# Kernel tuning notes

Measured on AMD Instinct MI355X. Metric: run time of the kernel, lower is better.

The kernel has to match this reference:

```python
import jax, jax.numpy as jnp
import numpy as np

DIM = 512
NUM_ITEM = 2048
K = 10


def setup_inputs() -> dict:
    key = jax.random.key(0)
    k1, k2, k3 = jax.random.split(key, 3)
    input1 = jax.random.normal(k1, (16, DIM, 32, 32), dtype=jnp.float32)
    input2 = jax.random.normal(k2, (16, DIM, 32, 32), dtype=jnp.float32)
    stdv = 1.0 / np.sqrt(DIM)
    mempool = jax.random.uniform(k3, (NUM_ITEM, DIM), minval=-stdv, maxval=stdv, dtype=jnp.float32)
    return {"input1": input1, "input2": input2, "mempool": mempool}


def _memorize(x, mempool):
    # x: [B, C, H, W] with C == DIM
    B, C, H, W = x.shape
    q = jnp.transpose(x, (0, 2, 3, 1)).reshape(-1, C)      # [N, C]
    att = jax.nn.softmax(q @ mempool.T, axis=1)            # [N, num_item]
    val, idx = jax.lax.top_k(att, K)                       # [N, K]
    val = jax.nn.softmax(val, axis=1)                      # renormalize top-k
    # scatter(val into zeros) @ mempool == gather rows of mempool and combine
    out = jnp.einsum('nk,nkd->nd', val, mempool[idx])      # [N, C]
    return jnp.transpose(out.reshape(B, H, W, C), (0, 3, 1, 2))


def reference(input1, input2, mempool):
    return (_memorize(input1, mempool), _memorize(input2, mempool))
```

## Files before the change

### kernel.cpp

```cpp
#include <hip/hip_runtime.h>
#include <math.h>

typedef __attribute__((ext_vector_type(4))) float f4;
typedef __attribute__((ext_vector_type(8))) _Float16 f16x8;
typedef __attribute__((ext_vector_type(8))) short bf16x8;
typedef __attribute__((ext_vector_type(4))) unsigned short u16x4;
typedef unsigned int u32;
typedef unsigned short u16;

#define DIMC  512
#define NITEM 2048
#define TK    10
#define WSP   (NITEM * DIMC)
#define XWSP  (32 * DIMC * 1024)
#define QWS_OFF (3 * WSP)

#define TPB    512
#define PXB    64
#define RIT    256
#define NRND   8
#define NSLICE 16

#define SSTR   66
#define MV_F 0
#define MI_F 5120
#define MM_F 10240
#define MS_F 10752
#define WB_F 11264
#define IB_F 11904

#define QB_SZ  12288
#define Q_PL   4096
#define LDS_BYTES 67584
#define KSWZ(i) (((i) ^ ((i) >> 2)) & 3)

union h16 { _Float16 h; u16 u; };

__device__ __forceinline__ u32 bf16_rne(float f) {
    u32 u = __float_as_uint(f);
    return (u + 0x7fffu + ((u >> 16) & 1u)) >> 16;
}

__device__ __forceinline__ void split3(float f, u16& ph, u16& pb, u16& pr) {
    h16 a; a.h = (_Float16)f;
    float f0 = (float)a.h;
    ph = a.u;
    pb = (u16)bf16_rne(f);
    pr = (u16)bf16_rne(f - f0);
}

__global__ __launch_bounds__(256)
void preconv_kernel(const float* __restrict__ mp, u16* __restrict__ ws)
{
    int idx = (blockIdx.x * 256 + threadIdx.x) * 4;
    int i  = idx >> 9;
    int k0 = idx & 511;
    f4 v = *(const f4*)(mp + (size_t)i * 512 + k0);
    int s  = k0 >> 5, kl = k0 & 31;
    int lh = (kl >> 2) & 3, pair = kl >> 4;
    u16x4 pH, pB, pR;
#pragma unroll
    for (int e = 0; e < 4; ++e) {
        u16 h, b, r; split3(v[e], h, b, r);
        pH[e] = h; pB[e] = b; pR[e] = r;
    }
    size_t base = (size_t)(i >> 4) * 8192 + (size_t)s * 512
                + (size_t)(lh * 16 + (i & 15)) * 8 + pair * 4;
    *(u16x4*)(ws + 0 * WSP + base) = pH;
    *(u16x4*)(ws + 1 * WSP + base) = pB;
    *(u16x4*)(ws + 2 * WSP + base) = pR;
}

__global__ __launch_bounds__(256)
void preconv_x_kernel(const float* __restrict__ x0, const float* __restrict__ x1,
                      u16* __restrict__ ws)
{
    int T   = blockIdx.x * 256 + threadIdx.x;
    int px  = T & 1023;
    int c4  = (T >> 10) & 127;
    int img = T >> 17;
    const float* x = (img < 16) ? x0 : x1;
    const float* src = x + ((size_t)(img & 15) * 512 + (size_t)c4 * 4) * 1024 + px;
    int s = c4 >> 3, pair = (c4 >> 2) & 1, lh = c4 & 3;
    u16x4 pH, pB, pR;
#pragma unroll
    for (int j = 0; j < 4; ++j) {
        u16 h, b, r; split3(src[(size_t)j * 1024], h, b, r);
        pH[j] = h; pB[j] = b; pR[j] = r;
    }
    size_t base = (size_t)QWS_OFF
                + (size_t)(img * 64 + (px >> 4)) * 8192 + (size_t)s * 512
                + (size_t)((lh * 16 + (px & 15)) << 3) + pair * 4;
    *(u16x4*)(ws + base + 0 * (size_t)XWSP) = pH;
    *(u16x4*)(ws + base + 1 * (size_t)XWSP) = pB;
    *(u16x4*)(ws + base + 2 * (size_t)XWSP) = pR;
}

__global__ __launch_bounds__(TPB, 4)
void memorize_direct(const float* __restrict__ mp, const u16* __restrict__ ws,
                     float* __restrict__ out)
{
    __shared__ float ldsf[16896];

    const int t    = threadIdx.x;
    const int lane = t & 63;
    const int w    = t >> 6;
    const int blk  = blockIdx.x;
    const int img  = blk >> 4;
    const int n0   = (blk & 15) * PXB;

    float* ob = out + (img < 16 ? (size_t)0 : (size_t)16 * DIMC * 1024)
                    + (size_t)(img & 15) * (DIMC * 1024);

    const int l15 = lane & 15;
    const int lh  = lane >> 4;
    const int ig  = w >> 1;
    const int pg  = w & 1;

    const int qp = t & 63;
    const int g  = t >> 6;

    float tv[TK]; int tix[TK];
#pragma unroll
    for (int q = 0; q < TK; ++q) { tv[q] = -INFINITY; tix[q] = 0x7fffffff; }
    float rm = -INFINITY, rs = 0.0f;

    const u16* aw = ws + (size_t)lane * 8 + (size_t)(ig * 4) * 8192;
    const int G0 = img * 64 + (blk & 15) * 4 + pg * 2;
    const u16* bw = ws + (size_t)QWS_OFF + (size_t)G0 * 8192 + (size_t)lane * 8;

#define ALOAD(IT, S)                                                           \
    {                                                                          \
        const u16* ap = ar + ((size_t)(IT) << 13) + ((S) << 9);                \
        aH[IT] = *(const f16x8*) (ap + 0 * WSP);                               \
        aB[IT] = *(const bf16x8*)(ap + 1 * WSP);                               \
        aR[IT] = *(const bf16x8*)(ap + 2 * WSP);                               \
    }

#pragma unroll 1
    for (int r = 0; r < NRND; ++r) {
        const u16* ar = aw + ((size_t)r << 17);
        f4 acc[4][2];
#pragma unroll
        for (int it = 0; it < 4; ++it)
#pragma unroll
            for (int pt = 0; pt < 2; ++pt) acc[it][pt] = (f4){0.f, 0.f, 0.f, 0.f};

#pragma unroll 1
        for (int s = 0; s < NSLICE; ++s) {
            f16x8 qH[2]; bf16x8 qB[2], qR[2];
#pragma unroll
            for (int pt = 0; pt < 2; ++pt) {
                const u16* bp = bw + ((size_t)pt << 13) + ((size_t)s << 9);
                qH[pt] = *(const f16x8*) (bp + 0 * (size_t)XWSP);
                qB[pt] = *(const bf16x8*)(bp + 1 * (size_t)XWSP);
                qR[pt] = *(const bf16x8*)(bp + 2 * (size_t)XWSP);
            }
            f16x8 aH[4]; bf16x8 aB[4], aR[4];
            ALOAD(0, s)
            ALOAD(1, s)
#pragma unroll
            for (int it = 0; it < 4; ++it) {
                if (it < 2) ALOAD(it + 2, s)
#pragma unroll
                for (int pt = 0; pt < 2; ++pt) {
                    f4 c = acc[it][pt];
                    c = __builtin_amdgcn_mfma_f32_16x16x32_f16 (aH[it], qH[pt], c, 0, 0, 0);
                    c = __builtin_amdgcn_mfma_f32_16x16x32_bf16(aB[it], qR[pt], c, 0, 0, 0);
                    c = __builtin_amdgcn_mfma_f32_16x16x32_bf16(aR[it], qB[pt], c, 0, 0, 0);
                    acc[it][pt] = c;
                }
            }
        }

        __syncthreads();
#pragma unroll
        for (int it = 0; it < 4; ++it) {
#pragma unroll
            for (int pt = 0; pt < 2; ++pt) {
                int row = (ig << 6) + (it << 4) + (lh << 2);
                int col = (pg << 5) + (pt << 4) + l15;
                float* sp = ldsf + row * SSTR + col;
                sp[0 * SSTR] = acc[it][pt][0];
                sp[1 * SSTR] = acc[it][pt][1];
                sp[2 * SSTR] = acc[it][pt][2];
                sp[3 * SSTR] = acc[it][pt][3];
            }
        }
        __syncthreads();

        float mloc = rm;
#pragma unroll 4
        for (int jj = 0; jj < 32; ++jj) {
            int   il = (g << 5) + jj;
            float v  = ldsf[il * SSTR + qp];
            mloc = fmaxf(mloc, v);
            if (v > tv[TK - 1]) {
                int   id = r * RIT + il;
                float cv = v; int ci = id;
#pragma unroll
                for (int q = 0; q < TK; ++q) {
                    bool  gt = cv > tv[q];
                    float nv = gt ? tv[q]  : cv;
                    int   ni = gt ? tix[q] : ci;
                    tv[q]  = gt ? cv : tv[q];
                    tix[q] = gt ? ci : tix[q];
                    cv = nv; ci = ni;
                }
            }
        }
        rs *= __expf(rm - mloc);
        rm = mloc;
#pragma unroll 4
        for (int jj = 0; jj < 32; ++jj) {
            int   il = (g << 5) + jj;
            float v  = ldsf[il * SSTR + qp];
            rs += __expf(v - rm);
        }
    }
#undef ALOAD

    __syncthreads();
    {
#pragma unroll
        for (int q = 0; q < TK; ++q) {
            ldsf[MV_F + (qp * 8 + g) * TK + q] = tv[q];
            ldsf[MI_F + (qp * 8 + g) * TK + q] = __int_as_float(tix[q]);
        }
        ldsf[MM_F + qp * 8 + g] = rm;
        ldsf[MS_F + qp * 8 + g] = rs;
    }
    __syncthreads();

    if (t < 64) {
        const int p = t;
        float gm[8], gs[8];
#pragma unroll
        for (int G = 0; G < 8; ++G) {
            gm[G] = ldsf[MM_F + p * 8 + G];
            gs[G] = ldsf[MS_F + p * 8 + G];
        }
        float mstar = gm[0];
#pragma unroll
        for (int G = 1; G < 8; ++G) mstar = fmaxf(mstar, gm[G]);
        float Z = 0.0f;
#pragma unroll
        for (int G = 0; G < 8; ++G) Z += gs[G] * __expf(gm[G] - mstar);

        int h0=0,h1=0,h2=0,h3=0,h4=0,h5=0,h6=0,h7=0;
        float ov[TK]; int oi[TK];
#pragma unroll
        for (int o = 0; o < TK; ++o) {
            float bv = -INFINITY; int bi = 0x7fffffff; int bg = 0;
#define SEL(G, HG)                                                               \
            {                                                                    \
                float v  = ldsf[MV_F + (p * 8 + G) * TK + (HG)];                 \
                int   id = __float_as_int(ldsf[MI_F + (p * 8 + G) * TK + (HG)]); \
                if (v > bv || (v == bv && id < bi)) { bv = v; bi = id; bg = G; } \
            }
            SEL(0, h0) SEL(1, h1) SEL(2, h2) SEL(3, h3)
            SEL(4, h4) SEL(5, h5) SEL(6, h6) SEL(7, h7)
#undef SEL
            ov[o] = bv; oi[o] = bi;
            h0 += (bg == 0); h1 += (bg == 1); h2 += (bg == 2); h3 += (bg == 3);
            h4 += (bg == 4); h5 += (bg == 5); h6 += (bg == 6); h7 += (bg == 7);
        }
        float pv[TK];
#pragma unroll
        for (int o = 0; o < TK; ++o) pv[o] = __expf(ov[o] - mstar) / Z;
        float pmax = pv[0];
        float wgt[TK]; float W = 0.0f;
#pragma unroll
        for (int o = 0; o < TK; ++o) { wgt[o] = __expf(pv[o] - pmax); W += wgt[o]; }
#pragma unroll
        for (int o = 0; o < TK; ++o) {
            ldsf[WB_F + p * TK + o] = wgt[o] / W;
            ldsf[IB_F + p * TK + o] = __int_as_float(oi[o]);
        }
    }
    __syncthreads();

    {
        const int ep = t & 63, cg = t >> 6;
        float wr[TK]; const float* rows[TK];
#pragma unroll
        for (int o = 0; o < TK; ++o) {
            wr[o]   = ldsf[WB_F + ep * TK + o];
            rows[o] = mp + (size_t)__float_as_int(ldsf[IB_F + ep * TK + o]) * DIMC;
        }
        float* obase = ob + n0 + ep;
#pragma unroll 4
        for (int cc = 0; cc < 16; ++cc) {
            int c = cg * 64 + cc * 4;
            f4 a = {0.0f, 0.0f, 0.0f, 0.0f};
#pragma unroll
            for (int o = 0; o < TK; ++o) {
                f4 rv = *(const f4*)(rows[o] + c);
#pragma unroll
                for (int z = 0; z < 4; ++z) a[z] = fmaf(wr[o], rv[z], a[z]);
            }
#pragma unroll
            for (int z = 0; z < 4; ++z) obase[(size_t)(c + z) * 1024] = a[z];
        }
    }
}

__global__ __launch_bounds__(TPB, 4)
void memorize_fb(const float* __restrict__ x0, const float* __restrict__ x1,
                 const float* __restrict__ mp, const u16* __restrict__ ws,
                 float* __restrict__ out)
{
    extern __shared__ char ldsb[];
    float* ldsf = (float*)ldsb;

    const int t    = threadIdx.x;
    const int lane = t & 63;
    const int w    = t >> 6;
    const int blk  = blockIdx.x;
    const int img  = blk >> 4;
    const int n0   = (blk & 15) * PXB;
    const int b    = img & 15;

    const float* x  = (img < 16) ? x0 : x1;
    const float* xb = x + (size_t)b * (DIMC * 1024);
    float* ob = out + (img < 16 ? (size_t)0 : (size_t)16 * DIMC * 1024)
                    + (size_t)b * (DIMC * 1024);

    const int l15 = lane & 15;
    const int lh  = lane >> 4;
    const int ksw = lh ^ KSWZ(l15);
    const int ig  = w >> 1;
    const int pg  = w & 1;
    const int qp = t & 63;
    const int g  = t >> 6;

    float tv[TK]; int tix[TK];
#pragma unroll
    for (int q = 0; q < TK; ++q) { tv[q] = -INFINITY; tix[q] = 0x7fffffff; }
    float rm = -INFINITY, rs = 0.0f;

    const int scl  = t & 31;
    const int spx  = (t >> 5) << 2;
    const int spos = (((scl >> 2) & 3) << 3) + ((scl >> 4) << 2) + (scl & 3);
    const int sslot = spos >> 3;
    const int soff  = (spos & 7) << 1;

    const u16* aw = ws + (size_t)lane * 8 + (size_t)(ig * 4) * 8192;
    const int qfb = (pg << 11) + (l15 << 6) + (ksw << 4);

#define STAGE_Q(S, BUF)                                                        \
    {                                                                          \
        const float* src = xb + (size_t)(((S) << 5) + scl) * 1024 + n0 + spx;  \
        f4 v = *(const f4*)src;                                                \
        _Pragma("unroll")                                                      \
        for (int e = 0; e < 4; ++e) {                                          \
            int px = spx + e;                                                  \
            u16 h, bb, rr; split3(v[e], h, bb, rr);                            \
            int ro = (BUF) * QB_SZ + (px << 6)                                 \
                   + (((sslot ^ KSWZ(px)) << 4) | soff);                       \
            *(u16*)(ldsb + ro)            = h;                                 \
            *(u16*)(ldsb + ro + Q_PL)     = bb;                                \
            *(u16*)(ldsb + ro + 2 * Q_PL) = rr;                                \
        }                                                                      \
    }

#define ALOADF(IT, S)                                                          \
    {                                                                          \
        const u16* ap = ar + ((size_t)(IT) << 13) + ((S) << 9);                \
        aH[IT] = *(const f16x8*) (ap + 0 * WSP);                               \
        aB[IT] = *(const bf16x8*)(ap + 1 * WSP);                               \
        aR[IT] = *(const bf16x8*)(ap + 2 * WSP);                               \
    }

#pragma unroll 1
    for (int r = 0; r < NRND; ++r) {
        const u16* ar = aw + ((size_t)r << 17);
        f4 acc[4][2];
#pragma unroll
        for (int it = 0; it < 4; ++it)
#pragma unroll
            for (int pt = 0; pt < 2; ++pt) acc[it][pt] = (f4){0.f, 0.f, 0.f, 0.f};

        __syncthreads();
        STAGE_Q(0, 0)
        __syncthreads();

#pragma unroll 1
        for (int s = 0; s < NSLICE; ++s) {
            const int cur = s & 1;
            f16x8 aH[4]; bf16x8 aB[4], aR[4];
            ALOADF(0, s)
            ALOADF(1, s)
            if (s + 1 < NSLICE) STAGE_Q(s + 1, cur ^ 1)

            const char* qc = ldsb + cur * QB_SZ + qfb;
            f16x8 qH[2]; bf16x8 qB[2], qR[2];
#pragma unroll
            for (int pt = 0; pt < 2; ++pt) {
                qH[pt] = *(const f16x8*) (qc + 0 * Q_PL + pt * 1024);
                qB[pt] = *(const bf16x8*)(qc + 1 * Q_PL + pt * 1024);
                qR[pt] = *(const bf16x8*)(qc + 2 * Q_PL + pt * 1024);
            }
#pragma unroll
            for (int it = 0; it < 4; ++it) {
                if (it < 2) ALOADF(it + 2, s)
#pragma unroll
                for (int pt = 0; pt < 2; ++pt) {
                    f4 c = acc[it][pt];
                    c = __builtin_amdgcn_mfma_f32_16x16x32_f16 (aH[it], qH[pt], c, 0, 0, 0);
                    c = __builtin_amdgcn_mfma_f32_16x16x32_bf16(aB[it], qR[pt], c, 0, 0, 0);
                    c = __builtin_amdgcn_mfma_f32_16x16x32_bf16(aR[it], qB[pt], c, 0, 0, 0);
                    acc[it][pt] = c;
                }
            }
            __syncthreads();
        }

#pragma unroll
        for (int it = 0; it < 4; ++it) {
#pragma unroll
            for (int pt = 0; pt < 2; ++pt) {
                int row = (ig << 6) + (it << 4) + (lh << 2);
                int col = (pg << 5) + (pt << 4) + l15;
                float* sp = ldsf + row * SSTR + col;
                sp[0 * SSTR] = acc[it][pt][0];
                sp[1 * SSTR] = acc[it][pt][1];
                sp[2 * SSTR] = acc[it][pt][2];
                sp[3 * SSTR] = acc[it][pt][3];
            }
        }
        __syncthreads();

        float mloc = rm;
#pragma unroll 4
        for (int jj = 0; jj < 32; ++jj) {
            int   il = (g << 5) + jj;
            float v  = ldsf[il * SSTR + qp];
            mloc = fmaxf(mloc, v);
            if (v > tv[TK - 1]) {
                int   id = r * RIT + il;
                float cv = v; int ci = id;
#pragma unroll
                for (int q = 0; q < TK; ++q) {
                    bool  gt = cv > tv[q];
                    float nv = gt ? tv[q]  : cv;
                    int   ni = gt ? tix[q] : ci;
                    tv[q]  = gt ? cv : tv[q];
                    tix[q] = gt ? ci : tix[q];
                    cv = nv; ci = ni;
                }
            }
        }
        rs *= __expf(rm - mloc);
        rm = mloc;
#pragma unroll 4
        for (int jj = 0; jj < 32; ++jj) {
            int   il = (g << 5) + jj;
            float v  = ldsf[il * SSTR + qp];
            rs += __expf(v - rm);
        }
    }
#undef STAGE_Q
#undef ALOADF

    __syncthreads();
    {
#pragma unroll
        for (int q = 0; q < TK; ++q) {
            ldsf[MV_F + (qp * 8 + g) * TK + q] = tv[q];
            ldsf[MI_F + (qp * 8 + g) * TK + q] = __int_as_float(tix[q]);
        }
        ldsf[MM_F + qp * 8 + g] = rm;
        ldsf[MS_F + qp * 8 + g] = rs;
    }
    __syncthreads();

    if (t < 64) {
        const int p = t;
        float gm[8], gs[8];
#pragma unroll
        for (int G = 0; G < 8; ++G) {
            gm[G] = ldsf[MM_F + p * 8 + G];
            gs[G] = ldsf[MS_F + p * 8 + G];
        }
        float mstar = gm[0];
#pragma unroll
        for (int G = 1; G < 8; ++G) mstar = fmaxf(mstar, gm[G]);
        float Z = 0.0f;
#pragma unroll
        for (int G = 0; G < 8; ++G) Z += gs[G] * __expf(gm[G] - mstar);

        int h0=0,h1=0,h2=0,h3=0,h4=0,h5=0,h6=0,h7=0;
        float ov[TK]; int oi[TK];
#pragma unroll
        for (int o = 0; o < TK; ++o) {
            float bv = -INFINITY; int bi = 0x7fffffff; int bg = 0;
#define SEL(G, HG)                                                               \
            {                                                                    \
                float v  = ldsf[MV_F + (p * 8 + G) * TK + (HG)];                 \
                int   id = __float_as_int(ldsf[MI_F + (p * 8 + G) * TK + (HG)]); \
                if (v > bv || (v == bv && id < bi)) { bv = v; bi = id; bg = G; } \
            }
            SEL(0, h0) SEL(1, h1) SEL(2, h2) SEL(3, h3)
            SEL(4, h4) SEL(5, h5) SEL(6, h6) SEL(7, h7)
#undef SEL
            ov[o] = bv; oi[o] = bi;
            h0 += (bg == 0); h1 += (bg == 1); h2 += (bg == 2); h3 += (bg == 3);
            h4 += (bg == 4); h5 += (bg == 5); h6 += (bg == 6); h7 += (bg == 7);
        }
        float pv[TK];
#pragma unroll
        for (int o = 0; o < TK; ++o) pv[o] = __expf(ov[o] - mstar) / Z;
        float pmax = pv[0];
        float wgt[TK]; float W = 0.0f;
#pragma unroll
        for (int o = 0; o < TK; ++o) { wgt[o] = __expf(pv[o] - pmax); W += wgt[o]; }
#pragma unroll
        for (int o = 0; o < TK; ++o) {
            ldsf[WB_F + p * TK + o] = wgt[o] / W;
            ldsf[IB_F + p * TK + o] = __int_as_float(oi[o]);
        }
    }
    __syncthreads();

    {
        const int ep = t & 63, cg = t >> 6;
        float wr[TK]; const float* rows[TK];
#pragma unroll
        for (int o = 0; o < TK; ++o) {
            wr[o]   = ldsf[WB_F + ep * TK + o];
            rows[o] = mp + (size_t)__float_as_int(ldsf[IB_F + ep * TK + o]) * DIMC;
        }
        float* obase = ob + n0 + ep;
#pragma unroll 4
        for (int cc = 0; cc < 16; ++cc) {
            int c = cg * 64 + cc * 4;
            f4 a = {0.0f, 0.0f, 0.0f, 0.0f};
#pragma unroll
            for (int o = 0; o < TK; ++o) {
                f4 rv = *(const f4*)(rows[o] + c);
#pragma unroll
                for (int z = 0; z < 4; ++z) a[z] = fmaf(wr[o], rv[z], a[z]);
            }
#pragma unroll
            for (int z = 0; z < 4; ++z) obase[(size_t)(c + z) * 1024] = a[z];
        }
    }
}

extern "C" void kernel_launch(void* const* d_in, const int* in_sizes, int n_in,
                              void* d_out, int out_size, void* d_ws, size_t ws_size,
                              hipStream_t stream) {
    const float* x0  = (const float*)d_in[0];
    const float* x1  = (const float*)d_in[1];
    const float* mpl = (const float*)d_in[2];
    float* out = (float*)d_out;
    u16* ws = (u16*)d_ws;

    const size_t ws_need = ((size_t)QWS_OFF + 3ull * (size_t)XWSP) * 2ull;

    preconv_kernel<<<dim3(1024), dim3(256), 0, stream>>>(mpl, ws);
    if (ws_size >= ws_need) {
        preconv_x_kernel<<<dim3(16384), dim3(256), 0, stream>>>(x0, x1, ws);
        memorize_direct<<<dim3(512), dim3(TPB), 0, stream>>>(mpl, ws, out);
    } else {
        memorize_fb<<<dim3(512), dim3(TPB), LDS_BYTES, stream>>>(x0, x1, mpl, ws, out);
    }
}
```

Baseline: 590.0 us.

## Stage mempool and query tiles in LDS via direct global-to-LDS loads

The main kernel stops having each wave load mempool and query fragments from global memory into registers. Each K-slice is now staged cooperatively into LDS with global_load_lds, using a swizzled layout, and fragments are read back from LDS for the MFMAs. Wave tiling changes from 4 item tiles x 2 pixel tiles per wave to 2 item tiles x 4 pixel tiles, so each wave covers all 64 pixels. The aim is less redundant global and L2 traffic, since waves now share mempool and query data. In exchange it adds two barriers per slice with no double buffering, so load latency is exposed, and it uses dynamic shared memory.

```diff
diff --git a/kernel.cpp b/kernel.cpp
--- a/kernel.cpp
+++ b/kernel.cpp
@@ -21,7 +21,11 @@
 #define NRND   8
 #define NSLICE 16
 
+#define MP_PL  16384
+#define Q_B    49152
+#define Q_PL   4096
 #define SSTR   66
+#define LDS_BYTES 67584
 #define MV_F 0
 #define MI_F 5120
 #define MM_F 10240
@@ -30,8 +34,7 @@
 #define IB_F 11904
 
 #define QB_SZ  12288
-#define Q_PL   4096
-#define LDS_BYTES 67584
+
 #define KSWZ(i) (((i) ^ ((i) >> 2)) & 3)
 
 union h16 { _Float16 h; u16 u; };
@@ -97,10 +100,11 @@
 }
 
 __global__ __launch_bounds__(TPB, 4)
-void memorize_direct(const float* __restrict__ mp, const u16* __restrict__ ws,
-                     float* __restrict__ out)
+void memorize_v11(const float* __restrict__ mp, const u16* __restrict__ ws,
+                  float* __restrict__ out)
 {
-    __shared__ float ldsf[16896];
+    extern __shared__ char ldsb[];
+    float* ldsf = (float*)ldsb;
 
     const int t    = threadIdx.x;
     const int lane = t & 63;
@@ -114,8 +118,7 @@
 
     const int l15 = lane & 15;
     const int lh  = lane >> 4;
-    const int ig  = w >> 1;
-    const int pg  = w & 1;
+    const int ksw = lh ^ KSWZ(l15);
 
     const int qp = t & 63;
     const int g  = t >> 6;
@@ -125,66 +128,87 @@
     for (int q = 0; q < TK; ++q) { tv[q] = -INFINITY; tix[q] = 0x7fffffff; }
     float rm = -INFINITY, rs = 0.0f;
 
-    const u16* aw = ws + (size_t)lane * 8 + (size_t)(ig * 4) * 8192;
-    const int G0 = img * 64 + (blk & 15) * 4 + pg * 2;
-    const u16* bw = ws + (size_t)QWS_OFF + (size_t)G0 * 8192 + (size_t)lane * 8;
-
-#define ALOAD(IT, S)                                                           \
-    {                                                                          \
-        const u16* ap = ar + ((size_t)(IT) << 13) + ((S) << 9);                \
-        aH[IT] = *(const f16x8*) (ap + 0 * WSP);                               \
-        aB[IT] = *(const bf16x8*)(ap + 1 * WSP);                               \
-        aR[IT] = *(const bf16x8*)(ap + 2 * WSP);                               \
-    }
+    const int permL = ((((lane & 3) ^ KSWZ(lane >> 2)) << 4) + (lane >> 2)) << 3;
+
+    const int Gx = img * 64 + (blk & 15) * 4 + w;
+    const u16* bsrc0 = ws + (size_t)QWS_OFF + ((size_t)Gx << 13) + permL;
+
+    const char* qb = ldsb + Q_B + (l15 << 6) + (ksw << 4);
+    const char* ab = ldsb + (size_t)((w << 5) + l15) * 64 + (ksw << 4);
 
 #pragma unroll 1
     for (int r = 0; r < NRND; ++r) {
-        const u16* ar = aw + ((size_t)r << 17);
-        f4 acc[4][2];
-#pragma unroll
-        for (int it = 0; it < 4; ++it)
-#pragma unroll
-            for (int pt = 0; pt < 2; ++pt) acc[it][pt] = (f4){0.f, 0.f, 0.f, 0.f};
+        f4 acc[2][4];
+#pragma unroll
+        for (int mt = 0; mt < 2; ++mt)
+#pragma unroll
+            for (int nt = 0; nt < 4; ++nt) acc[mt][nt] = (f4){0.f, 0.f, 0.f, 0.f};
 
 #pragma unroll 1
         for (int s = 0; s < NSLICE; ++s) {
-            f16x8 qH[2]; bf16x8 qB[2], qR[2];
-#pragma unroll
-            for (int pt = 0; pt < 2; ++pt) {
-                const u16* bp = bw + ((size_t)pt << 13) + ((size_t)s << 9);
-                qH[pt] = *(const f16x8*) (bp + 0 * (size_t)XWSP);
-                qB[pt] = *(const bf16x8*)(bp + 1 * (size_t)XWSP);
-                qR[pt] = *(const bf16x8*)(bp + 2 * (size_t)XWSP);
-            }
-            f16x8 aH[4]; bf16x8 aB[4], aR[4];
-            ALOAD(0, s)
-            ALOAD(1, s)
-#pragma unroll
-            for (int it = 0; it < 4; ++it) {
-                if (it < 2) ALOAD(it + 2, s)
-#pragma unroll
-                for (int pt = 0; pt < 2; ++pt) {
-                    f4 c = acc[it][pt];
-                    c = __builtin_amdgcn_mfma_f32_16x16x32_f16 (aH[it], qH[pt], c, 0, 0, 0);
-                    c = __builtin_amdgcn_mfma_f32_16x16x32_bf16(aB[it], qR[pt], c, 0, 0, 0);
-                    c = __builtin_amdgcn_mfma_f32_16x16x32_bf16(aR[it], qB[pt], c, 0, 0, 0);
-                    acc[it][pt] = c;
+            __syncthreads();
+
+#pragma unroll
+            for (int p = 0; p < 3; ++p) {
+#pragma unroll
+                for (int gg = 0; gg < 2; ++gg) {
+                    const u16* src = ws + (size_t)p * WSP
+                                   + ((size_t)(r * 16 + w * 2 + gg) << 13)
+                                   + (s << 9) + permL;
+                    char* dst = ldsb + p * MP_PL + ((w << 5) + (gg << 4)) * 64;
+                    __builtin_amdgcn_global_load_lds(
+                        (const __attribute__((address_space(1))) u32*)src,
+                        (__attribute__((address_space(3))) u32*)dst, 16, 0, 0);
                 }
             }
+            if (w < 4) {
+#pragma unroll
+                for (int p = 0; p < 3; ++p) {
+                    const u16* src = bsrc0 + (size_t)p * XWSP + (s << 9);
+                    char* dst = ldsb + Q_B + p * Q_PL + (w << 10);
+                    __builtin_amdgcn_global_load_lds(
+                        (const __attribute__((address_space(1))) u32*)src,
+                        (__attribute__((address_space(3))) u32*)dst, 16, 0, 0);
+                }
+            }
+            __syncthreads();
+
+            f16x8  bqH[4];
+            bf16x8 bqB[4], bqR[4];
+#pragma unroll
+            for (int nt = 0; nt < 4; ++nt) {
+                bqH[nt] = *(const f16x8*) (qb + 0 * Q_PL + nt * 1024);
+                bqB[nt] = *(const bf16x8*)(qb + 1 * Q_PL + nt * 1024);
+                bqR[nt] = *(const bf16x8*)(qb + 2 * Q_PL + nt * 1024);
+            }
+#pragma unroll
+            for (int mt = 0; mt < 2; ++mt) {
+                f16x8  aH = *(const f16x8*) (ab + 0 * MP_PL + mt * 1024);
+                bf16x8 aB = *(const bf16x8*)(ab + 1 * MP_PL + mt * 1024);
+                bf16x8 aR = *(const bf16x8*)(ab + 2 * MP_PL + mt * 1024);
+#pragma unroll
+                for (int nt = 0; nt < 4; ++nt) {
+                    f4 c = acc[mt][nt];
+                    c = __builtin_amdgcn_mfma_f32_16x16x32_f16 (aH, bqH[nt], c, 0, 0, 0);
+                    c = __builtin_amdgcn_mfma_f32_16x16x32_bf16(aB, bqR[nt], c, 0, 0, 0);
+                    c = __builtin_amdgcn_mfma_f32_16x16x32_bf16(aR, bqB[nt], c, 0, 0, 0);
+                    acc[mt][nt] = c;
+                }
+            }
         }
 
         __syncthreads();
 #pragma unroll
-        for (int it = 0; it < 4; ++it) {
-#pragma unroll
-            for (int pt = 0; pt < 2; ++pt) {
-                int row = (ig << 6) + (it << 4) + (lh << 2);
-                int col = (pg << 5) + (pt << 4) + l15;
+        for (int mt = 0; mt < 2; ++mt) {
+#pragma unroll
+            for (int nt = 0; nt < 4; ++nt) {
+                int row = (w << 5) + (mt << 4) + (lh << 2);
+                int col = (nt << 4) + l15;
                 float* sp = ldsf + row * SSTR + col;
-                sp[0 * SSTR] = acc[it][pt][0];
-                sp[1 * SSTR] = acc[it][pt][1];
-                sp[2 * SSTR] = acc[it][pt][2];
-                sp[3 * SSTR] = acc[it][pt][3];
+                sp[0 * SSTR] = acc[mt][nt][0];
+                sp[1 * SSTR] = acc[mt][nt][1];
+                sp[2 * SSTR] = acc[mt][nt][2];
+                sp[3 * SSTR] = acc[mt][nt][3];
             }
         }
         __syncthreads();
@@ -218,7 +242,6 @@
             rs += __expf(v - rm);
         }
     }
-#undef ALOAD
 
     __syncthreads();
     {
@@ -562,7 +585,7 @@
     preconv_kernel<<<dim3(1024), dim3(256), 0, stream>>>(mpl, ws);
     if (ws_size >= ws_need) {
         preconv_x_kernel<<<dim3(16384), dim3(256), 0, stream>>>(x0, x1, ws);
-        memorize_direct<<<dim3(512), dim3(TPB), 0, stream>>>(mpl, ws, out);
+        memorize_v11<<<dim3(512), dim3(TPB), LDS_BYTES, stream>>>(mpl, ws, out);
     } else {
         memorize_fb<<<dim3(512), dim3(TPB), LDS_BYTES, stream>>>(x0, x1, mpl, ws, out);
     }
```

Measured after the change: 612.9 us. +3.9%, slower.
